# Performance work log

Measured on AMD Instinct MI355X. Metric: run time of the kernel, lower is better.

The kernel has to match this reference:

```python
import math
import jax, jax.numpy as jnp
import numpy as np

N, L, C, H, R = 4, 1024, 1024, 16, 8
HD = C // H
LORA_SCALE = 16.0 / 8.0          # alpha / rank
LOGIT_SCALE_MAX = math.log(100.0)
EPS = 1e-12                      # F.normalize eps


def setup_inputs() -> dict:
    key = jax.random.key(0)
    ks = jax.random.split(key, 10)
    return {
        "x": jax.random.normal(ks[0], (N, L, C), jnp.float32),
        "in_proj_weight": jax.random.normal(ks[1], (3 * C, C), jnp.float32) * 0.02,
        "in_proj_bias": jnp.zeros((3 * C,), jnp.float32),
        "lora_A_q": jax.random.normal(ks[2], (R, C), jnp.float32) * 0.02,
        "lora_B_q": jax.random.normal(ks[3], (C, R), jnp.float32) * 0.02,
        "lora_A_k": jax.random.normal(ks[4], (R, C), jnp.float32) * 0.02,
        "lora_B_k": jax.random.normal(ks[5], (C, R), jnp.float32) * 0.02,
        "lora_A_v": jax.random.normal(ks[6], (R, C), jnp.float32) * 0.02,
        "lora_B_v": jax.random.normal(ks[7], (C, R), jnp.float32) * 0.02,
        "logit_scale": jnp.full((H, 1, 1), math.log(10.0), jnp.float32),
        "out_proj_weight": jax.random.normal(ks[8], (C, C), jnp.float32) * 0.02,
        "out_proj_bias": jnp.zeros((C,), jnp.float32),
    }


def _l2norm(t):
    # matches F.normalize(dim=-1): x / max(||x||, eps)
    n = jnp.sqrt(jnp.sum(t * t, axis=-1, keepdims=True))
    return t / jnp.maximum(n, EPS)


def reference(x, in_proj_weight, in_proj_bias,
              lora_A_q, lora_B_q, lora_A_k, lora_B_k, lora_A_v, lora_B_v,
              logit_scale, out_proj_weight, out_proj_bias):
    # fused QKV projection (frozen base weights)
    qkv = jnp.einsum('nlc,oc->nlo', x, in_proj_weight) + in_proj_bias  # [N,L,3C]
    q0, k0, v0 = jnp.split(qkv, 3, axis=-1)

    # low-rank LoRA adapters: (x A^T) B^T * scale
    def lora(A, B):
        return jnp.einsum('nlr,cr->nlc', jnp.einsum('nlc,rc->nlr', x, A), B) * LORA_SCALE

    q = q0 + lora(lora_A_q, lora_B_q)
    k = k0 + lora(lora_A_k, lora_B_k)
    v = v0 + lora(lora_A_v, lora_B_v)

    # [N,L,C] -> [N,H,L,HD]
    def heads(t):
        return t.reshape(N, L, H, HD).transpose(0, 2, 1, 3)

    q, k, v = heads(q), heads(k), heads(v)

    # cosine-similarity attention with clamped learnable per-head logit scale
    attn = jnp.einsum('nhld,nhmd->nhlm', _l2norm(q), _l2norm(k))
    scale = jnp.exp(jnp.minimum(logit_scale, LOGIT_SCALE_MAX))  # [H,1,1]
    attn = jax.nn.softmax(attn * scale, axis=-1)

    out = jnp.einsum('nhlm,nhmd->nhld', attn, v)  # [N,H,L,HD]
    out = out.transpose(0, 2, 1, 3).reshape(N, L, C)

    return jnp.einsum('nlc,oc->nlo', out, out_proj_weight) + out_proj_bias
```

## Files before the change

### kernel.cpp

```cpp
#include <hip/hip_runtime.h>
#include <hip/hip_bf16.h>
#include <cstdint>
#include <cstddef>

#define DEVI __device__ __forceinline__

typedef __attribute__((ext_vector_type(8))) short bf16x8;
typedef __attribute__((ext_vector_type(4))) float f32x4;
typedef __attribute__((ext_vector_type(8))) unsigned short u16x8;

DEVI unsigned short f2bf(float f) {
  union { float f; unsigned int u; } v; v.f = f;
  unsigned int r = v.u + 0x7FFFu + ((v.u >> 16) & 1u);
  return (unsigned short)(r >> 16);
}

DEVI void gload_lds16(const void* g, void* l) {
  __builtin_amdgcn_global_load_lds((const __attribute__((address_space(1))) void*)g,
                                   (__attribute__((address_space(3))) void*)l,
                                   16, 0, 0);
}

__global__ void cvt_k(const float* __restrict__ in, unsigned short* __restrict__ out, int n4) {
  int i = blockIdx.x * 256 + threadIdx.x;
  if (i >= n4) return;
  float4 v = reinterpret_cast<const float4*>(in)[i];
  ushort4 o;
  o.x = f2bf(v.x); o.y = f2bf(v.y); o.z = f2bf(v.z); o.w = f2bf(v.w);
  reinterpret_cast<ushort4*>(out)[i] = o;
}

__global__ void weff_k(const float* __restrict__ W,
                       const float* __restrict__ Aq, const float* __restrict__ Bq,
                       const float* __restrict__ Ak, const float* __restrict__ Bk,
                       const float* __restrict__ Av, const float* __restrict__ Bv,
                       unsigned short* __restrict__ out) {
  int idx = blockIdx.x * 256 + threadIdx.x;
  int o = idx >> 10, c = idx & 1023;
  const float* A; const float* B; int ol;
  if (o < 1024)      { A = Aq; B = Bq; ol = o; }
  else if (o < 2048) { A = Ak; B = Bk; ol = o - 1024; }
  else               { A = Av; B = Bv; ol = o - 2048; }
  float acc = W[idx];
#pragma unroll
  for (int r = 0; r < 8; ++r) acc += 2.0f * B[ol*8 + r] * A[r*1024 + c];
  out[idx] = f2bf(acc);
}

template<int NCOLS, int EPI>
__global__ __launch_bounds__(256)
void gemm_k(const unsigned short* __restrict__ A,
            const unsigned short* __restrict__ Bw,
            const float* __restrict__ bias,
            unsigned short* __restrict__ q_out,
            unsigned short* __restrict__ k_out,
            unsigned short* __restrict__ v_out,
            float* __restrict__ f_out)
{
  constexpr int K = 1024;
  constexpr int NBN = NCOLS / 128;
  __shared__ unsigned short As[128*32];
  __shared__ unsigned short Bs[128*32];
  const int bid  = blockIdx.x;
  const int bn   = bid % NBN, bm = bid / NBN;
  const int tid  = threadIdx.x;
  const int lane = tid & 63, wave = tid >> 6;
  const int wr = wave >> 1, wc = wave & 1;
  const int l15 = lane & 15, g = lane >> 4;

  const f32x4 fzero = {0.f, 0.f, 0.f, 0.f};
  f32x4 acc[4][4];
#pragma unroll
  for (int m = 0; m < 4; ++m)
#pragma unroll
    for (int n = 0; n < 4; ++n) acc[m][n] = fzero;

  for (int k0 = 0; k0 < K; k0 += 32) {
#pragma unroll
    for (int j = 0; j < 2; ++j) {
      int off = j*4096 + tid*16;
      int r = off >> 6, cb = off & 63;
      gload_lds16((const char*)(A  + (size_t)(bm*128 + r) * K) + k0*2 + cb, (char*)As + off);
      gload_lds16((const char*)(Bw + (size_t)(bn*128 + r) * K) + k0*2 + cb, (char*)Bs + off);
    }
    __syncthreads();
    bf16x8 af[4], bfr[4];
#pragma unroll
    for (int m = 0; m < 4; ++m)
      af[m] = *(const bf16x8*)((const char*)As + (wr*64 + m*16 + l15)*64 + g*16);
#pragma unroll
    for (int n = 0; n < 4; ++n)
      bfr[n] = *(const bf16x8*)((const char*)Bs + (wc*64 + n*16 + l15)*64 + g*16);
#pragma unroll
    for (int m = 0; m < 4; ++m)
#pragma unroll
      for (int n = 0; n < 4; ++n)
        acc[m][n] = __builtin_amdgcn_mfma_f32_16x16x32_bf16(af[m], bfr[n], acc[m][n], 0, 0, 0);
    __syncthreads();
  }

  const int colBase = bn*128 + wc*64;
  const int rBase   = bm*128 + wr*64;
  float bias_n[4];
#pragma unroll
  for (int n = 0; n < 4; ++n) bias_n[n] = bias[colBase + n*16 + l15];
#pragma unroll
  for (int m = 0; m < 4; ++m)
#pragma unroll
    for (int n = 0; n < 4; ++n)
#pragma unroll
      for (int r = 0; r < 4; ++r) acc[m][n][r] += bias_n[n];

  if constexpr (EPI == 0) {
    const int sec = colBase >> 10;
    if (sec < 2) {
#pragma unroll
      for (int m = 0; m < 4; ++m)
#pragma unroll
        for (int r = 0; r < 4; ++r) {
          float ss = 0.f;
#pragma unroll
          for (int n = 0; n < 4; ++n) { float x = acc[m][n][r]; ss += x*x; }
          ss += __shfl_xor(ss, 1);
          ss += __shfl_xor(ss, 2);
          ss += __shfl_xor(ss, 4);
          ss += __shfl_xor(ss, 8);
          float inv = 1.0f / fmaxf(sqrtf(ss), 1e-12f);
#pragma unroll
          for (int n = 0; n < 4; ++n) acc[m][n][r] *= inv;
        }
    }
    unsigned short* dst = (sec == 0) ? q_out : ((sec == 1) ? k_out : v_out);
    const int h = (colBase & 1023) >> 6;
#pragma unroll
    for (int m = 0; m < 4; ++m)
#pragma unroll
      for (int r = 0; r < 4; ++r) {
        int mrow = rBase + m*16 + g*4 + r;
        int nidx = mrow >> 10, li = mrow & 1023;
        size_t base = (((size_t)(nidx*16 + h))*1024 + li)*64;
#pragma unroll
        for (int n = 0; n < 4; ++n)
          dst[base + n*16 + l15] = f2bf(acc[m][n][r]);
      }
  } else {
#pragma unroll
    for (int m = 0; m < 4; ++m)
#pragma unroll
      for (int r = 0; r < 4; ++r) {
        int mrow = rBase + m*16 + g*4 + r;
#pragma unroll
        for (int n = 0; n < 4; ++n)
          f_out[(size_t)mrow*NCOLS + colBase + n*16 + l15] = acc[m][n][r];
      }
  }
}

__global__ __launch_bounds__(256)
void attn_k(const unsigned short* __restrict__ qh,
            const unsigned short* __restrict__ kh,
            const unsigned short* __restrict__ vh,
            const float* __restrict__ logit_scale,
            unsigned short* __restrict__ ao)
{
  __shared__ unsigned short Ks [64*64];
  __shared__ unsigned short VTs[64*64];
  __shared__ unsigned short Ps [4][16*64];
  const int bid = blockIdx.x;
  const int xcd = bid & 7, slot = bid >> 3;
  const int nh = xcd + ((slot >> 4) << 3);
  const int qb = slot & 15;
  const int h = nh & 15;
  const int tid = threadIdx.x;
  const int w = tid >> 6, lane = tid & 63;
  const int l15 = lane & 15, g = lane >> 4;
  const float s = __expf(fminf(logit_scale[h], 4.6051701859880914f));

  const unsigned short* Qb = qh + ((size_t)nh*1024 + qb*64) * 64;
  const unsigned short* Kb = kh + (size_t)nh * 1024 * 64;
  const unsigned short* Vb = vh + (size_t)nh * 1024 * 64;

  bf16x8 qf[2];
#pragma unroll
  for (int kk = 0; kk < 2; ++kk)
    qf[kk] = *(const bf16x8*)(Qb + (w*16 + l15)*64 + kk*32 + g*8);

  const f32x4 fzero = {0.f, 0.f, 0.f, 0.f};
  f32x4 oacc[4];
#pragma unroll
  for (int n = 0; n < 4; ++n) oacc[n] = fzero;
  float rs[4] = {0.f, 0.f, 0.f, 0.f};

  for (int kt = 0; kt < 16; ++kt) {
#pragma unroll
    for (int j = 0; j < 2; ++j) {
      int off = j*4096 + tid*16;
      int r = off >> 7, cbyte = off & 127;
      int scb = cbyte ^ ((r & 7) << 4);
      gload_lds16((const char*)(Kb + (size_t)(kt*64 + r) * 64) + scb, (char*)Ks + off);
    }
#pragma unroll
    for (int j2 = 0; j2 < 2; ++j2) {
      int k  = (tid >> 3) + j2*32;
      int d0 = (tid & 7) * 8;
      u16x8 v = *(const u16x8*)(Vb + (size_t)(kt*64 + k) * 64 + d0);
#pragma unroll
      for (int e = 0; e < 8; ++e) {
        int row = d0 + e;
        int sw = ((row ^ (row >> 3)) & 7) << 4;
        *(unsigned short*)((char*)VTs + row*128 + ((k*2) ^ sw)) = v[e];
      }
    }
    __syncthreads();

    f32x4 sf[4];
#pragma unroll
    for (int n = 0; n < 4; ++n) sf[n] = fzero;
#pragma unroll
    for (int n = 0; n < 4; ++n) {
      int krow = n*16 + l15;
      int sw = (krow & 7) << 4;
#pragma unroll
      for (int kk = 0; kk < 2; ++kk) {
        bf16x8 bfr = *(const bf16x8*)((const char*)Ks + krow*128 + ((kk*64 + g*16) ^ sw));
        sf[n] = __builtin_amdgcn_mfma_f32_16x16x32_bf16(qf[kk], bfr, sf[n], 0, 0, 0);
      }
    }

#pragma unroll
    for (int n = 0; n < 4; ++n)
#pragma unroll
      for (int r = 0; r < 4; ++r) {
        float p = __expf(s * sf[n][r]);
        rs[r] += p;
        int prow = g*4 + r;
        int swp = ((prow >> 2) & 3) << 5;
        *(unsigned short*)((char*)Ps[w] + prow*128 + (((n*16 + l15)*2) ^ swp)) = f2bf(p);
      }

#pragma unroll
    for (int kk = 0; kk < 2; ++kk) {
      int swp = ((l15 >> 2) & 3) << 5;
      bf16x8 af = *(const bf16x8*)((const char*)Ps[w] + l15*128 + ((kk*64 + g*16) ^ swp));
#pragma unroll
      for (int n = 0; n < 4; ++n) {
        int vrow = n*16 + l15;
        int swv = ((vrow ^ (vrow >> 3)) & 7) << 4;
        bf16x8 bfv = *(const bf16x8*)((const char*)VTs + vrow*128 + ((kk*64 + g*16) ^ swv));
        oacc[n] = __builtin_amdgcn_mfma_f32_16x16x32_bf16(af, bfv, oacc[n], 0, 0, 0);
      }
    }
    __syncthreads();
  }

#pragma unroll
  for (int r = 0; r < 4; ++r) {
    rs[r] += __shfl_xor(rs[r], 1);
    rs[r] += __shfl_xor(rs[r], 2);
    rs[r] += __shfl_xor(rs[r], 4);
    rs[r] += __shfl_xor(rs[r], 8);
  }
  const int nidx = nh >> 4;
#pragma unroll
  for (int r = 0; r < 4; ++r) {
    float inv = 1.0f / rs[r];
    int qrow = qb*64 + w*16 + g*4 + r;
    size_t rowoff = (size_t)(nidx*1024 + qrow) * 1024 + h*64;
#pragma unroll
    for (int n = 0; n < 4; ++n)
      ao[rowoff + n*16 + l15] = f2bf(oacc[n][r] * inv);
  }
}

extern "C" void kernel_launch(void* const* d_in, const int* in_sizes, int n_in,
                              void* d_out, int out_size, void* d_ws, size_t ws_size,
                              hipStream_t stream) {
  const float* x    = (const float*)d_in[0];
  const float* Wqkv = (const float*)d_in[1];
  const float* bqkv = (const float*)d_in[2];
  const float* Aq   = (const float*)d_in[3];
  const float* Bq   = (const float*)d_in[4];
  const float* Ak   = (const float*)d_in[5];
  const float* Bk   = (const float*)d_in[6];
  const float* Av   = (const float*)d_in[7];
  const float* Bv   = (const float*)d_in[8];
  const float* ls   = (const float*)d_in[9];
  const float* Wout = (const float*)d_in[10];
  const float* bout = (const float*)d_in[11];
  float* out = (float*)d_out;

  char* ws = (char*)d_ws;
  unsigned short* xb   = (unsigned short*)(ws);
  unsigned short* weff = (unsigned short*)(ws + (8u  << 20));
  unsigned short* wob  = (unsigned short*)(ws + (14u << 20));
  unsigned short* qhp  = (unsigned short*)(ws + (16u << 20));
  unsigned short* khp  = (unsigned short*)(ws + (24u << 20));
  unsigned short* vhp  = (unsigned short*)(ws + (32u << 20));
  unsigned short* aop  = xb;

  cvt_k <<<4096, 256, 0, stream>>>(x, xb, 1048576);
  cvt_k <<<1024, 256, 0, stream>>>(Wout, wob, 262144);
  weff_k<<<12288, 256, 0, stream>>>(Wqkv, Aq, Bq, Ak, Bk, Av, Bv, weff);

  gemm_k<3072, 0><<<768, 256, 0, stream>>>(xb, weff, bqkv, qhp, khp, vhp, nullptr);
  attn_k<<<1024, 256, 0, stream>>>(qhp, khp, vhp, ls, aop);
  gemm_k<1024, 1><<<256, 256, 0, stream>>>(aop, wob, bout, nullptr, nullptr, nullptr, out);
}
```

Measured before the change: 203.0 us.

## Write V pre-transposed from QKV GEMM and double-buffer K/V loads in attention

The QKV GEMM epilogue now writes V transposed per head ([d][l]). It stages tiles through shared memory so the global stores are 16-byte coalesced rows. Because V arrives pre-transposed, the attention kernel loads both K and V^T with async global-to-LDS copies instead of a register transpose and scalar LDS stores. It also double-buffers those tiles so the next tile's load overlaps the current tile's MFMA work. In exchange it uses more LDS per attention block, adds syncs in the GEMM epilogue, and depends on reusing the As/Bs tiles safely.

```diff
diff --git a/kernel.cpp b/kernel.cpp
--- a/kernel.cpp
+++ b/kernel.cpp
@@ -113,6 +113,7 @@
 
   if constexpr (EPI == 0) {
     const int sec = colBase >> 10;
+    const int h = (colBase & 1023) >> 6;
     if (sec < 2) {
 #pragma unroll
       for (int m = 0; m < 4; ++m)
@@ -129,20 +130,47 @@
 #pragma unroll
           for (int n = 0; n < 4; ++n) acc[m][n][r] *= inv;
         }
+      unsigned short* dst = (sec == 0) ? q_out : k_out;
+#pragma unroll
+      for (int m = 0; m < 4; ++m)
+#pragma unroll
+        for (int r = 0; r < 4; ++r) {
+          int mrow = rBase + m*16 + g*4 + r;
+          int nidx = mrow >> 10, li = mrow & 1023;
+          size_t base = (((size_t)(nidx*16 + h))*1024 + li)*64;
+#pragma unroll
+          for (int n = 0; n < 4; ++n)
+            dst[base + n*16 + l15] = f2bf(acc[m][n][r]);
+        }
+    } else {
+      unsigned short* pool = (wave & 1) ? Bs : As;
+      const int nidx = rBase >> 10;
+      const size_t gbase = ((size_t)(nidx*16 + h) * 64) * 1024 + (rBase & 1023);
+#pragma unroll
+      for (int round = 0; round < 2; ++round) {
+        if ((wave >> 1) == round) {
+#pragma unroll
+          for (int m = 0; m < 4; ++m)
+#pragma unroll
+            for (int n = 0; n < 4; ++n) {
+              ushort4 pk;
+              pk.x = f2bf(acc[m][n][0]); pk.y = f2bf(acc[m][n][1]);
+              pk.z = f2bf(acc[m][n][2]); pk.w = f2bf(acc[m][n][3]);
+              int d_loc = n*16 + l15;
+              int li    = m*16 + g*4;
+              *(ushort4*)((char*)pool + d_loc*128 + ((li*2) ^ ((d_loc & 7) << 4))) = pk;
+            }
+#pragma unroll
+          for (int p = 0; p < 8; ++p) {
+            int d_loc = p*8 + (lane >> 3);
+            int lic   = (lane & 7) * 8;
+            u16x8 row = *(const u16x8*)((const char*)pool + d_loc*128 + ((lic*2) ^ ((d_loc & 7) << 4)));
+            *(u16x8*)(v_out + gbase + (size_t)d_loc*1024 + lic) = row;
+          }
+        }
+        __syncthreads();
+      }
     }
-    unsigned short* dst = (sec == 0) ? q_out : ((sec == 1) ? k_out : v_out);
-    const int h = (colBase & 1023) >> 6;
-#pragma unroll
-    for (int m = 0; m < 4; ++m)
-#pragma unroll
-      for (int r = 0; r < 4; ++r) {
-        int mrow = rBase + m*16 + g*4 + r;
-        int nidx = mrow >> 10, li = mrow & 1023;
-        size_t base = (((size_t)(nidx*16 + h))*1024 + li)*64;
-#pragma unroll
-        for (int n = 0; n < 4; ++n)
-          dst[base + n*16 + l15] = f2bf(acc[m][n][r]);
-      }
   } else {
 #pragma unroll
     for (int m = 0; m < 4; ++m)
@@ -159,13 +187,13 @@
 __global__ __launch_bounds__(256)
 void attn_k(const unsigned short* __restrict__ qh,
             const unsigned short* __restrict__ kh,
-            const unsigned short* __restrict__ vh,
+            const unsigned short* __restrict__ vt,
             const float* __restrict__ logit_scale,
             unsigned short* __restrict__ ao)
 {
-  __shared__ unsigned short Ks [64*64];
-  __shared__ unsigned short VTs[64*64];
-  __shared__ unsigned short Ps [4][16*64];
+  __shared__ unsigned short Ks [2][4096];
+  __shared__ unsigned short VTs[2][4096];
+  __shared__ unsigned short Ps [4][1024];
   const int bid = blockIdx.x;
   const int xcd = bid & 7, slot = bid >> 3;
   const int nh = xcd + ((slot >> 4) << 3);
@@ -176,9 +204,9 @@
   const int l15 = lane & 15, g = lane >> 4;
   const float s = __expf(fminf(logit_scale[h], 4.6051701859880914f));
 
-  const unsigned short* Qb = qh + ((size_t)nh*1024 + qb*64) * 64;
-  const unsigned short* Kb = kh + (size_t)nh * 1024 * 64;
-  const unsigned short* Vb = vh + (size_t)nh * 1024 * 64;
+  const unsigned short* Qb  = qh + ((size_t)nh*1024 + qb*64) * 64;
+  const unsigned short* Kb  = kh + (size_t)nh * 1024 * 64;
+  const unsigned short* Vtb = vt + (size_t)nh * 64 * 1024;
 
   bf16x8 qf[2];
 #pragma unroll
@@ -191,27 +219,26 @@
   for (int n = 0; n < 4; ++n) oacc[n] = fzero;
   float rs[4] = {0.f, 0.f, 0.f, 0.f};
 
+#define STAGE(b, kt)                                                              \
+  {                                                                               \
+    _Pragma("unroll")                                                             \
+    for (int j = 0; j < 2; ++j) {                                                 \
+      int off = j*4096 + tid*16;                                                  \
+      int r = off >> 7, cb = off & 127;                                           \
+      int scb = cb ^ ((r & 7) << 4);                                              \
+      gload_lds16((const char*)Kb  + (size_t)((kt)*64 + r)*128 + scb,             \
+                  (char*)Ks[b] + off);                                            \
+      gload_lds16((const char*)Vtb + (size_t)r*2048 + (kt)*128 + scb,             \
+                  (char*)VTs[b] + off);                                           \
+    }                                                                             \
+  }
+
+  STAGE(0, 0);
+  __syncthreads();
+
   for (int kt = 0; kt < 16; ++kt) {
-#pragma unroll
-    for (int j = 0; j < 2; ++j) {
-      int off = j*4096 + tid*16;
-      int r = off >> 7, cbyte = off & 127;
-      int scb = cbyte ^ ((r & 7) << 4);
-      gload_lds16((const char*)(Kb + (size_t)(kt*64 + r) * 64) + scb, (char*)Ks + off);
-    }
-#pragma unroll
-    for (int j2 = 0; j2 < 2; ++j2) {
-      int k  = (tid >> 3) + j2*32;
-      int d0 = (tid & 7) * 8;
-      u16x8 v = *(const u16x8*)(Vb + (size_t)(kt*64 + k) * 64 + d0);
-#pragma unroll
-      for (int e = 0; e < 8; ++e) {
-        int row = d0 + e;
-        int sw = ((row ^ (row >> 3)) & 7) << 4;
-        *(unsigned short*)((char*)VTs + row*128 + ((k*2) ^ sw)) = v[e];
-      }
-    }
-    __syncthreads();
+    const int cur = kt & 1;
+    if (kt < 15) STAGE(cur ^ 1, kt + 1);
 
     f32x4 sf[4];
 #pragma unroll
@@ -222,7 +249,7 @@
       int sw = (krow & 7) << 4;
 #pragma unroll
       for (int kk = 0; kk < 2; ++kk) {
-        bf16x8 bfr = *(const bf16x8*)((const char*)Ks + krow*128 + ((kk*64 + g*16) ^ sw));
+        bf16x8 bfr = *(const bf16x8*)((const char*)Ks[cur] + krow*128 + ((kk*64 + g*16) ^ sw));
         sf[n] = __builtin_amdgcn_mfma_f32_16x16x32_bf16(qf[kk], bfr, sf[n], 0, 0, 0);
       }
     }
@@ -245,13 +272,13 @@
 #pragma unroll
       for (int n = 0; n < 4; ++n) {
         int vrow = n*16 + l15;
-        int swv = ((vrow ^ (vrow >> 3)) & 7) << 4;
-        bf16x8 bfv = *(const bf16x8*)((const char*)VTs + vrow*128 + ((kk*64 + g*16) ^ swv));
+        bf16x8 bfv = *(const bf16x8*)((const char*)VTs[cur] + vrow*128 + ((kk*64 + g*16) ^ ((vrow & 7) << 4)));
         oacc[n] = __builtin_amdgcn_mfma_f32_16x16x32_bf16(af, bfv, oacc[n], 0, 0, 0);
       }
     }
     __syncthreads();
   }
+#undef STAGE
 
 #pragma unroll
   for (int r = 0; r < 4; ++r) {
@@ -295,14 +322,14 @@
   unsigned short* wob  = (unsigned short*)(ws + (14u << 20));
   unsigned short* qhp  = (unsigned short*)(ws + (16u << 20));
   unsigned short* khp  = (unsigned short*)(ws + (24u << 20));
-  unsigned short* vhp  = (unsigned short*)(ws + (32u << 20));
+  unsigned short* vtp  = (unsigned short*)(ws + (32u << 20));
   unsigned short* aop  = xb;
 
   cvt_k <<<4096, 256, 0, stream>>>(x, xb, 1048576);
   cvt_k <<<1024, 256, 0, stream>>>(Wout, wob, 262144);
   weff_k<<<12288, 256, 0, stream>>>(Wqkv, Aq, Bq, Ak, Bk, Av, Bv, weff);
 
-  gemm_k<3072, 0><<<768, 256, 0, stream>>>(xb, weff, bqkv, qhp, khp, vhp, nullptr);
-  attn_k<<<1024, 256, 0, stream>>>(qhp, khp, vhp, ls, aop);
+  gemm_k<3072, 0><<<768, 256, 0, stream>>>(xb, weff, bqkv, qhp, khp, vtp, nullptr);
+  attn_k<<<1024, 256, 0, stream>>>(qhp, khp, vtp, ls, aop);
   gemm_k<1024, 1><<<256, 256, 0, stream>>>(aop, wob, bout, nullptr, nullptr, nullptr, out);
 }
```

New measurement: 215.0 us. 6.0% more time.
